# Kernel tuning notes

Hardware: AMD Instinct MI355X
Metric: run time of the kernel (lower is better)

The kernel has to match this reference:

```python
import jax, jax.numpy as jnp
import numpy as np

B, C_IN, C_OUT, N = 4096, 256, 256, 25


def setup_inputs() -> dict:
    key = jax.random.key(0)
    k_x, k_adj, k_w, k_b = jax.random.split(key, 4)
    x = jax.random.normal(k_x, (B, C_IN, N), dtype=jnp.float32)
    adj = jax.random.uniform(k_adj, (N, N), dtype=jnp.float32)
    # Conv1d(C_in, C_out, 1) weight is [C_out, C_in, 1]; drop trailing 1.
    W = jax.random.normal(k_w, (C_OUT, C_IN), dtype=jnp.float32) * (1.0 / np.sqrt(C_IN))
    b = jax.random.normal(k_b, (C_OUT,), dtype=jnp.float32) * 0.01
    return {"x": x, "adj": adj, "W": W, "b": b}


def reference(x, adj, W, b):
    # 1x1 Conv1d == per-node linear transform: [B, C_out, N]
    support = jnp.einsum('oc,bcn->bon', W, x) + b[None, :, None]
    # Dense adjacency aggregation: support @ adj.T -> [B, C_out, N]
    output = jnp.einsum('bon,mn->bom', support, adj)
    # dropout=0 (disabled); in_features == out_features -> identity residual
    return jax.nn.relu(output + x)
```

## Files before the change

kernel.cpp:

```cpp
#include <hip/hip_runtime.h>
#include <hip/hip_bf16.h>


#define BATCH 4096
#define C 256
#define N 25
#define NB 8
#define XW 6400
#define YSTR 264

typedef __bf16 bf16x8 __attribute__((ext_vector_type(8)));
typedef float f32x4 __attribute__((ext_vector_type(4)));

#define GLOAD16(gp, lp)                                                        \
    __builtin_amdgcn_global_load_lds(                                          \
        (const __attribute__((address_space(1))) unsigned int*)(gp),           \
        (__attribute__((address_space(3))) unsigned int*)(lp), 16, 0, 0)

__global__ void prep_kernel(const float* __restrict__ W, const float* __restrict__ adj,
                            bf16x8* __restrict__ Wshuf, float* __restrict__ adjS) {
    int i = blockIdx.x * 256 + threadIdx.x;
    int f = i >> 6, l = i & 63;
    int T = f >> 3, kk = f & 7;
    int quad = l >> 4, l15 = l & 15;
    int o = T * 16 + l15;
    int cb = kk * 32 + quad * 8;
    bf16x8 v;
    #pragma unroll
    for (int j = 0; j < 8; ++j) v[j] = (__bf16)W[o * C + cb + j];
    Wshuf[i] = v;
    if (blockIdx.x == 0 && threadIdx.x < 32) {
        float s = 0.f;
        if (threadIdx.x < N)
            for (int n = 0; n < N; ++n) s += adj[threadIdx.x * N + n];
        adjS[threadIdx.x] = s;
    }
}

__global__ __launch_bounds__(512, 4) void gcn_kernel(
    const float* __restrict__ x, const float* __restrict__ adj,
    const float* __restrict__ bias, const float* __restrict__ adjSg,
    const bf16x8* __restrict__ Wshuf, float* __restrict__ out)
{
    __shared__ __align__(16) float  xs2[2][XW];
    __shared__ __align__(16) float  outS[XW];
    __shared__ __align__(16) __bf16 adjbf[32 * 40];
    __shared__ float biasS[C];
    __bf16* const ys = (__bf16*)outS;

    const int tid = threadIdx.x;
    const int wv = tid >> 6, lane = tid & 63;
    const int quad = lane >> 4, l15 = lane & 15;
    const int o0 = wv * 32;
    const int b0 = blockIdx.x * NB;

    for (int e = tid; e < N * N; e += 512) {
        int m = e / N, n = e - m * N;
        adjbf[m * 40 + n] = (__bf16)adj[e];
    }
    if (tid < N) {
        #pragma unroll
        for (int n = N; n < 32; ++n) adjbf[tid * 40 + n] = (__bf16)0.f;
    } else if (tid < 32) {
        #pragma unroll
        for (int n = 0; n < 32; ++n) adjbf[tid * 40 + n] = (__bf16)0.f;
    }
    if (tid < C) biasS[tid] = bias[tid];

    bf16x8 af[8][2];
    #pragma unroll
    for (int kk = 0; kk < 8; ++kk)
        #pragma unroll
        for (int ot = 0; ot < 2; ++ot)
            af[kk][ot] = Wshuf[(((wv * 2 + ot) * 8 + kk) << 6) + lane];

    const float aS0 = adjSg[l15];
    const float aS1 = adjSg[16 + l15];

    __syncthreads();

    const bf16x8 a0 = *(const bf16x8*)&adjbf[l15 * 40 + quad * 8];
    const bf16x8 a1 = *(const bf16x8*)&adjbf[(16 + l15) * 40 + quad * 8];

    {
        const float4* xb = (const float4*)(x + (size_t)b0 * XW);
        #pragma unroll
        for (int rr = 0; rr < 4; ++rr)
            if (rr < 3 || lane < 8)
                GLOAD16(xb + (wv * 200 + rr * 64 + lane),
                        &xs2[0][(wv * 200 + rr * 64) * 4]);
    }

    #pragma unroll 1
    for (int bi = 0; bi < NB; ++bi) {
        const int cur = bi & 1;
        float* outb = out + (size_t)(b0 + bi) * XW;
        const bool pf = (bi + 1 < NB);

        if (pf) {
            const float4* xb = (const float4*)(x + (size_t)(b0 + bi + 1) * XW);
            #pragma unroll
            for (int rr = 0; rr < 4; ++rr)
                if (rr < 3 || lane < 8)
                    GLOAD16(xb + (wv * 200 + rr * 64 + lane),
                            &xs2[cur ^ 1][(wv * 200 + rr * 64) * 4]);
        }

        if (bi == 0 || !pf) asm volatile("s_waitcnt vmcnt(4)" ::: "memory");
        else                asm volatile("s_waitcnt vmcnt(8)" ::: "memory");

        const float* xc = xs2[cur];

        #pragma unroll
        for (int ctl = 0; ctl < 2; ++ctl) {
            const int c = o0 + ctl * 16 + l15;
            const float* xr = xc + c * N;
            bf16x8 xf;
            if (quad < 3) {
                #pragma unroll
                for (int j = 0; j < 8; ++j) xf[j] = (__bf16)xr[quad * 8 + j];
            } else {
                xf[0] = (__bf16)xr[24];
                #pragma unroll
                for (int j = 1; j < 8; ++j) xf[j] = (__bf16)0.f;
            }
            f32x4 y0 = __builtin_amdgcn_mfma_f32_16x16x32_bf16(a0, xf, (f32x4)0.f, 0, 0, 0);
            f32x4 y1 = __builtin_amdgcn_mfma_f32_16x16x32_bf16(a1, xf, (f32x4)0.f, 0, 0, 0);
            #pragma unroll
            for (int r2 = 0; r2 < 4; ++r2) {
                ys[(quad * 4 + r2) * YSTR + c]      = (__bf16)y0[r2];
                ys[(16 + quad * 4 + r2) * YSTR + c] = (__bf16)y1[r2];
            }
        }
        asm volatile("s_waitcnt lgkmcnt(0)\n\ts_barrier" ::: "memory");

        f32x4 acc[2][2];
        #pragma unroll
        for (int ot = 0; ot < 2; ++ot) { acc[ot][0] = (f32x4)0.f; acc[ot][1] = (f32x4)0.f; }
        #pragma unroll
        for (int kk = 0; kk < 8; ++kk) {
            bf16x8 bfr0 = *(const bf16x8*)&ys[l15 * YSTR + kk * 32 + quad * 8];
            bf16x8 bfr1 = *(const bf16x8*)&ys[(16 + l15) * YSTR + kk * 32 + quad * 8];
            #pragma unroll
            for (int ot = 0; ot < 2; ++ot) {
                acc[ot][0] = __builtin_amdgcn_mfma_f32_16x16x32_bf16(af[kk][ot], bfr0, acc[ot][0], 0, 0, 0);
                acc[ot][1] = __builtin_amdgcn_mfma_f32_16x16x32_bf16(af[kk][ot], bfr1, acc[ot][1], 0, 0, 0);
            }
        }
        asm volatile("s_barrier" ::: "memory");

        #pragma unroll
        for (int ot = 0; ot < 2; ++ot)
            #pragma unroll
            for (int r2 = 0; r2 < 4; ++r2) {
                const int o = o0 + ot * 16 + quad * 4 + r2;
                const float bia = biasS[o];
                {
                    const int m = l15;
                    float v = acc[ot][0][r2] + bia * aS0 + xc[o * N + m];
                    outS[o * N + m] = v > 0.f ? v : 0.f;
                }
                if (l15 < N - 16) {
                    const int m = 16 + l15;
                    float v = acc[ot][1][r2] + bia * aS1 + xc[o * N + m];
                    outS[o * N + m] = v > 0.f ? v : 0.f;
                }
            }

        #pragma unroll
        for (int rr = 0; rr < 4; ++rr)
            if (rr < 3 || lane < 8) {
                int i4 = wv * 200 + rr * 64 + lane;
                ((float4*)outb)[i4] = ((const float4*)outS)[i4];
            }

        asm volatile("s_barrier" ::: "memory");
    }
}

extern "C" void kernel_launch(void* const* d_in, const int* in_sizes, int n_in,
                              void* d_out, int out_size, void* d_ws, size_t ws_size,
                              hipStream_t stream) {
    (void)in_sizes; (void)n_in; (void)out_size; (void)ws_size;
    const float* x    = (const float*)d_in[0];
    const float* adj  = (const float*)d_in[1];
    const float* W    = (const float*)d_in[2];
    const float* bias = (const float*)d_in[3];
    float* out = (float*)d_out;

    unsigned char* ws = (unsigned char*)d_ws;
    bf16x8* Wshuf = (bf16x8*)ws;
    float*  adjS  = (float*)(ws + 131072);

    prep_kernel<<<32, 256, 0, stream>>>(W, adj, Wshuf, adjS);
    gcn_kernel<<<BATCH / NB, 512, 0, stream>>>(x, adj, bias, adjS, Wshuf, out);
}
```

Measured before the change: 204.5 us.

## Software-pipeline aggregation ahead of GEMM with double-buffered ys and direct output stores

Restructures the per-batch loop so the adjacency aggregation for the next batch element runs after the current GEMM, using double-buffered bf16 ys buffers. x prefetch goes two elements ahead into the buffer just consumed. The LDS output staging buffer is removed, so results are written straight to global memory with scalar stores. The goal is fewer barriers per iteration and more overlap, at the cost of uncoalesced 4-byte global stores and trickier vmcnt accounting.

```diff
diff --git a/kernel.cpp b/kernel.cpp
--- a/kernel.cpp
+++ b/kernel.cpp
@@ -8,6 +8,8 @@
 #define NB 8
 #define XW 6400
 #define YSTR 264
+#define YROWS 25
+#define YBUF (YROWS * YSTR)
 
 typedef __bf16 bf16x8 __attribute__((ext_vector_type(8)));
 typedef float f32x4 __attribute__((ext_vector_type(4)));
@@ -43,10 +45,9 @@
     const bf16x8* __restrict__ Wshuf, float* __restrict__ out)
 {
     __shared__ __align__(16) float  xs2[2][XW];
-    __shared__ __align__(16) float  outS[XW];
-    __shared__ __align__(16) __bf16 adjbf[32 * 40];
+    __shared__ __align__(16) __bf16 ys2[2][YBUF];
     __shared__ float biasS[C];
-    __bf16* const ys = (__bf16*)outS;
+    __bf16* const adjbf = &ys2[0][0];
 
     const int tid = threadIdx.x;
     const int wv = tid >> 6, lane = tid & 63;
@@ -54,16 +55,9 @@
     const int o0 = wv * 32;
     const int b0 = blockIdx.x * NB;
 
-    for (int e = tid; e < N * N; e += 512) {
-        int m = e / N, n = e - m * N;
-        adjbf[m * 40 + n] = (__bf16)adj[e];
-    }
-    if (tid < N) {
-        #pragma unroll
-        for (int n = N; n < 32; ++n) adjbf[tid * 40 + n] = (__bf16)0.f;
-    } else if (tid < 32) {
-        #pragma unroll
-        for (int n = 0; n < 32; ++n) adjbf[tid * 40 + n] = (__bf16)0.f;
+    for (int e = tid; e < 32 * 32; e += 512) {
+        int m = e >> 5, n = e & 31;
+        adjbf[m * 40 + n] = (m < N && n < N) ? (__bf16)adj[m * N + n] : (__bf16)0.f;
     }
     if (tid < C) biasS[tid] = bias[tid];
 
@@ -79,38 +73,27 @@
 
     __syncthreads();
 
+    {
+        const float4* xb0 = (const float4*)(x + (size_t)b0 * XW);
+        const float4* xb1 = (const float4*)(x + (size_t)(b0 + 1) * XW);
+        #pragma unroll
+        for (int rr = 0; rr < 4; ++rr)
+            if (rr < 3 || lane < 8)
+                GLOAD16(xb0 + (wv * 200 + rr * 64 + lane),
+                        &xs2[0][(wv * 200 + rr * 64) * 4]);
+        #pragma unroll
+        for (int rr = 0; rr < 4; ++rr)
+            if (rr < 3 || lane < 8)
+                GLOAD16(xb1 + (wv * 200 + rr * 64 + lane),
+                        &xs2[1][(wv * 200 + rr * 64) * 4]);
+    }
+
     const bf16x8 a0 = *(const bf16x8*)&adjbf[l15 * 40 + quad * 8];
     const bf16x8 a1 = *(const bf16x8*)&adjbf[(16 + l15) * 40 + quad * 8];
-
-    {
-        const float4* xb = (const float4*)(x + (size_t)b0 * XW);
-        #pragma unroll
-        for (int rr = 0; rr < 4; ++rr)
-            if (rr < 3 || lane < 8)
-                GLOAD16(xb + (wv * 200 + rr * 64 + lane),
-                        &xs2[0][(wv * 200 + rr * 64) * 4]);
-    }
-
-    #pragma unroll 1
-    for (int bi = 0; bi < NB; ++bi) {
-        const int cur = bi & 1;
-        float* outb = out + (size_t)(b0 + bi) * XW;
-        const bool pf = (bi + 1 < NB);
-
-        if (pf) {
-            const float4* xb = (const float4*)(x + (size_t)(b0 + bi + 1) * XW);
-            #pragma unroll
-            for (int rr = 0; rr < 4; ++rr)
-                if (rr < 3 || lane < 8)
-                    GLOAD16(xb + (wv * 200 + rr * 64 + lane),
-                            &xs2[cur ^ 1][(wv * 200 + rr * 64) * 4]);
-        }
-
-        if (bi == 0 || !pf) asm volatile("s_waitcnt vmcnt(4)" ::: "memory");
-        else                asm volatile("s_waitcnt vmcnt(8)" ::: "memory");
-
-        const float* xc = xs2[cur];
-
+    asm volatile("s_waitcnt lgkmcnt(0)" ::: "memory");
+    __builtin_amdgcn_s_barrier();
+
+    auto AGG = [&](const float* xc, __bf16* ysw) {
         #pragma unroll
         for (int ctl = 0; ctl < 2; ++ctl) {
             const int c = o0 + ctl * 16 + l15;
@@ -128,53 +111,83 @@
             f32x4 y1 = __builtin_amdgcn_mfma_f32_16x16x32_bf16(a1, xf, (f32x4)0.f, 0, 0, 0);
             #pragma unroll
             for (int r2 = 0; r2 < 4; ++r2) {
-                ys[(quad * 4 + r2) * YSTR + c]      = (__bf16)y0[r2];
-                ys[(16 + quad * 4 + r2) * YSTR + c] = (__bf16)y1[r2];
+                ysw[(quad * 4 + r2) * YSTR + c] = (__bf16)y0[r2];
+                if (quad * 4 + r2 < 9)
+                    ysw[(16 + quad * 4 + r2) * YSTR + c] = (__bf16)y1[r2];
             }
         }
-        asm volatile("s_waitcnt lgkmcnt(0)\n\ts_barrier" ::: "memory");
+    };
+
+    asm volatile("s_waitcnt vmcnt(4)" ::: "memory");
+    AGG(xs2[0], ys2[0]);
+    asm volatile("s_waitcnt lgkmcnt(0)" ::: "memory");
+    __builtin_amdgcn_s_barrier();
+
+    const int row1 = (l15 < 9) ? (16 + l15) : 24;
+
+    #pragma unroll 1
+    for (int bi = 0; bi < NB; ++bi) {
+        const int cur = bi & 1;
+        const float* xc = xs2[cur];
+        const __bf16* ysr = ys2[cur];
+        float* outb = out + (size_t)(b0 + bi) * XW;
+
+        if (bi == 0)          asm volatile("s_waitcnt vmcnt(0)" ::: "memory");
+        else if (bi < NB - 1) asm volatile("s_waitcnt vmcnt(16)" ::: "memory");
 
         f32x4 acc[2][2];
         #pragma unroll
         for (int ot = 0; ot < 2; ++ot) { acc[ot][0] = (f32x4)0.f; acc[ot][1] = (f32x4)0.f; }
         #pragma unroll
         for (int kk = 0; kk < 8; ++kk) {
-            bf16x8 bfr0 = *(const bf16x8*)&ys[l15 * YSTR + kk * 32 + quad * 8];
-            bf16x8 bfr1 = *(const bf16x8*)&ys[(16 + l15) * YSTR + kk * 32 + quad * 8];
+            bf16x8 bfr0 = *(const bf16x8*)&ysr[l15  * YSTR + kk * 32 + quad * 8];
+            bf16x8 bfr1 = *(const bf16x8*)&ysr[row1 * YSTR + kk * 32 + quad * 8];
             #pragma unroll
             for (int ot = 0; ot < 2; ++ot) {
                 acc[ot][0] = __builtin_amdgcn_mfma_f32_16x16x32_bf16(af[kk][ot], bfr0, acc[ot][0], 0, 0, 0);
                 acc[ot][1] = __builtin_amdgcn_mfma_f32_16x16x32_bf16(af[kk][ot], bfr1, acc[ot][1], 0, 0, 0);
             }
         }
-        asm volatile("s_barrier" ::: "memory");
-
+
+        float ov0[2][4], ov1[2][4];
         #pragma unroll
         for (int ot = 0; ot < 2; ++ot)
             #pragma unroll
             for (int r2 = 0; r2 < 4; ++r2) {
                 const int o = o0 + ot * 16 + quad * 4 + r2;
                 const float bia = biasS[o];
-                {
-                    const int m = l15;
-                    float v = acc[ot][0][r2] + bia * aS0 + xc[o * N + m];
-                    outS[o * N + m] = v > 0.f ? v : 0.f;
-                }
-                if (l15 < N - 16) {
-                    const int m = 16 + l15;
-                    float v = acc[ot][1][r2] + bia * aS1 + xc[o * N + m];
-                    outS[o * N + m] = v > 0.f ? v : 0.f;
-                }
-            }
-
-        #pragma unroll
-        for (int rr = 0; rr < 4; ++rr)
-            if (rr < 3 || lane < 8) {
-                int i4 = wv * 200 + rr * 64 + lane;
-                ((float4*)outb)[i4] = ((const float4*)outS)[i4];
-            }
-
-        asm volatile("s_barrier" ::: "memory");
+                float v0 = acc[ot][0][r2] + bia * aS0 + xc[o * N + l15];
+                ov0[ot][r2] = v0 > 0.f ? v0 : 0.f;
+                float xr1 = (l15 < 9) ? xc[o * N + 16 + l15] : 0.f;
+                float v1 = acc[ot][1][r2] + bia * aS1 + xr1;
+                ov1[ot][r2] = v1 > 0.f ? v1 : 0.f;
+            }
+
+        asm volatile("s_waitcnt lgkmcnt(0)" ::: "memory");
+
+        if (bi + 2 < NB) {
+            const float4* xb = (const float4*)(x + (size_t)(b0 + bi + 2) * XW);
+            #pragma unroll
+            for (int rr = 0; rr < 4; ++rr)
+                if (rr < 3 || lane < 8)
+                    GLOAD16(xb + (wv * 200 + rr * 64 + lane),
+                            &xs2[cur][(wv * 200 + rr * 64) * 4]);
+        }
+
+        #pragma unroll
+        for (int ot = 0; ot < 2; ++ot)
+            #pragma unroll
+            for (int r2 = 0; r2 < 4; ++r2) {
+                const int o = o0 + ot * 16 + quad * 4 + r2;
+                outb[o * N + l15] = ov0[ot][r2];
+                if (l15 < 9) outb[o * N + 16 + l15] = ov1[ot][r2];
+            }
+
+        if (bi + 1 < NB)
+            AGG(xs2[cur ^ 1], ys2[cur ^ 1]);
+
+        asm volatile("s_waitcnt lgkmcnt(0)" ::: "memory");
+        __builtin_amdgcn_s_barrier();
     }
 }
 
```

Result: slower. 302.4 us (+47.9%).
